# Optimization experiments

Measured on AMD Instinct MI355X. Metric: run time of the kernel, lower is better.

The kernel has to match this reference:

```python
import jax, jax.numpy as jnp
import numpy as np

B, T, D = 2, 2048, 2048
H, HKV, RD = 16, 4, 64
DH = D // H          # 128
REP = H // HKV       # 4
NEG = -1e30


def _apply_rope(x, cos, sin, rd):
    # x: (B, h, T, Dh); cos/sin: (T, rd//2) broadcast over (B, h)
    xr, xp = x[..., :rd], x[..., rd:]
    x1, x2 = xr[..., ::2], xr[..., 1::2]
    rot = jnp.stack([x1 * cos - x2 * sin, x1 * sin + x2 * cos], axis=-1)
    rot = rot.reshape(x1.shape[:-1] + (rd,))
    return jnp.concatenate([rot, xp], axis=-1)


def setup_inputs() -> dict:
    key = jax.random.key(0)
    ks = jax.random.split(key, 6)
    x = jax.random.normal(ks[0], (B, T, D), dtype=jnp.float32)
    # rotary tables for the first RD dims (RD//2 frequency pairs)
    inv_freq = 1.0 / (10000.0 ** (np.arange(RD // 2, dtype=np.float32) / (RD // 2)))
    ang = np.arange(T, dtype=np.float32)[:, None] * inv_freq[None, :]  # (T, RD//2)
    cos = jnp.asarray(np.cos(ang), dtype=jnp.float32)
    sin = jnp.asarray(np.sin(ang), dtype=jnp.float32)
    s = 0.02
    Wq = jax.random.normal(ks[1], (H * DH, D), dtype=jnp.float32) * s
    Wk = jax.random.normal(ks[2], (HKV * DH, D), dtype=jnp.float32) * s
    Wv = jax.random.normal(ks[3], (HKV * DH, D), dtype=jnp.float32) * s
    Wo = jax.random.normal(ks[4], (D, D), dtype=jnp.float32) * s
    temp = jnp.full((H,), 1.0 / np.sqrt(DH), dtype=jnp.float32)
    return {"x": x, "cos": cos, "sin": sin, "Wq": Wq, "Wk": Wk, "Wv": Wv, "Wo": Wo, "temp": temp}


def reference(x, cos, sin, Wq, Wk, Wv, Wo, temp):
    Bt, Tt, _ = x.shape
    q = (x @ Wq.T).reshape(Bt, Tt, H, DH).transpose(0, 2, 1, 3)    # (B,H,T,Dh)
    k = (x @ Wk.T).reshape(Bt, Tt, HKV, DH).transpose(0, 2, 1, 3)  # (B,Hkv,T,Dh)
    v = (x @ Wv.T).reshape(Bt, Tt, HKV, DH).transpose(0, 2, 1, 3)
    k = jnp.repeat(k, REP, axis=1)  # GQA repeat_interleave -> (B,H,T,Dh)
    v = jnp.repeat(v, REP, axis=1)
    q = _apply_rope(q, cos, sin, RD)
    k = _apply_rope(k, cos, sin, RD)
    q = q * temp[None, :, None, None]
    # SDPA causal, with default 1/sqrt(Dh) scale on top of learned temp
    scores = jnp.einsum("bhqd,bhkd->bhqk", q, k) / np.sqrt(DH)
    causal = jnp.tril(jnp.ones((Tt, Tt), dtype=bool))
    scores = jnp.where(causal[None, None], scores, NEG)
    attn = jax.nn.softmax(scores, axis=-1)
    out = jnp.einsum("bhqk,bhkd->bhqd", attn, v)  # (B,H,T,Dh)
    out = out.transpose(0, 2, 1, 3).reshape(Bt, Tt, H * DH)
    return out @ Wo.T
```

## Files before the change

kernel.cpp:

```cpp
#include <hip/hip_runtime.h>
#include <hip/hip_bf16.h>
#include <math.h>

#define B_   2
#define T_   2048
#define D_   2048
#define H_   16
#define HKV_ 4
#define DH_  128
#define RD_  64
#define KD_  (HKV_ * DH_)
#define SQKV 3072
#define VOFF 2560

typedef __attribute__((ext_vector_type(8))) short  short8;
typedef __attribute__((ext_vector_type(4))) short  short4v;
typedef __attribute__((ext_vector_type(4))) float  floatx4;

__device__ __forceinline__ void async16(const __hip_bfloat16* g, __hip_bfloat16* l) {
  __builtin_amdgcn_global_load_lds(
      (const __attribute__((address_space(1))) void*)g,
      (__attribute__((address_space(3))) void*)l, 16, 0, 0);
}

__device__ __forceinline__ short bf16b(float x) {
  union { __hip_bfloat16 h; short s; } u;
  u.h = __float2bfloat16(x);
  return u.s;
}

struct ConvArgs {
  const float* src[5];
  __hip_bfloat16* dst[5];
  int n[5];
};

__global__ __launch_bounds__(256) void conv_bf16(ConvArgs a) {
  const int arr = blockIdx.y;
  const int i = (blockIdx.x * 256 + threadIdx.x) * 8;
  if (i >= a.n[arr]) return;
  const float4 f1 = *(const float4*)(a.src[arr] + i);
  const float4 f2 = *(const float4*)(a.src[arr] + i + 4);
  union { short8 v; __hip_bfloat16 h[8]; } o;
  o.h[0] = __float2bfloat16(f1.x); o.h[1] = __float2bfloat16(f1.y);
  o.h[2] = __float2bfloat16(f1.z); o.h[3] = __float2bfloat16(f1.w);
  o.h[4] = __float2bfloat16(f2.x); o.h[5] = __float2bfloat16(f2.y);
  o.h[6] = __float2bfloat16(f2.z); o.h[7] = __float2bfloat16(f2.w);
  *(short8*)(a.dst[arr] + i) = o.v;
}

template <int MODE>
__global__ __launch_bounds__(512, 2) void gemm_192(const __hip_bfloat16* __restrict__ A,
                                                   const __hip_bfloat16* __restrict__ Bw,
                                                   void* __restrict__ Cout,
                                                   __hip_bfloat16* __restrict__ vtout,
                                                   int M, int N, int K, int nwg_x) {
  __shared__ __hip_bfloat16 ABs[2][28 * 512];

  const int tid  = threadIdx.x;
  const int lane = tid & 63;
  const int w    = tid >> 6;
  const int wm   = w >> 2, wn = w & 3;
  const int quad = lane >> 4, m16 = lane & 15;

  const int nwg = gridDim.x;
  const int q8  = nwg >> 3, r8 = nwg & 7;
  const int xcd = blockIdx.x & 7, o8 = blockIdx.x >> 3;
  const int swz = (xcd < r8 ? xcd * (q8 + 1) : r8 * (q8 + 1) + (xcd - r8) * q8) + o8;
  const int bx = swz % nwg_x, by = swz / nwg_x;
  const int bm = by * 256, bn = bx * 192;

  const __hip_bfloat16* gp[4];
  int lp[4];
  if (w < 7) {
#pragma unroll
    for (int e = 0; e < 4; ++e) {
      const int p = w * 4 + e;
      lp[e] = p * 512;
      if (p < 16) gp[e] = A  + (size_t)(bm + p * 16 + m16) * K + quad * 8;
      else        gp[e] = Bw + (size_t)(bn + (p - 16) * 16 + m16) * K + quad * 8;
    }
  }

  const int nt = K >> 5;

  if (w < 7) {
#pragma unroll
    for (int e = 0; e < 4; ++e) async16(gp[e], &ABs[0][lp[e]]);
  }

  floatx4 acc[8][3] = {};
  const int fragoff = (quad * 16 + m16) * 8;

  for (int t = 0; t < nt; ++t) {
    const int cur = t & 1, stg = cur ^ 1;
    asm volatile("s_waitcnt vmcnt(0)" ::: "memory");
    __builtin_amdgcn_s_barrier();
    __builtin_amdgcn_sched_barrier(0);

    const __hip_bfloat16* base = &ABs[cur][0];
    const bool doStage = (w < 7) && (t + 1 < nt);
    const size_t ko = (size_t)(t + 1) * 32;

    short8 a0[4], b[3];
#pragma unroll
    for (int i = 0; i < 4; ++i)
      a0[i] = *(const short8*)(base + (wm * 8 + i) * 512 + fragoff);
#pragma unroll
    for (int j = 0; j < 3; ++j)
      b[j] = *(const short8*)(base + (16 + wn * 3 + j) * 512 + fragoff);
    if (doStage) {
      async16(gp[0] + ko, &ABs[stg][lp[0]]);
      async16(gp[1] + ko, &ABs[stg][lp[1]]);
    }
    __builtin_amdgcn_s_barrier();
    __builtin_amdgcn_sched_barrier(0);
    __builtin_amdgcn_s_setprio(1);
#pragma unroll
    for (int i = 0; i < 4; ++i)
#pragma unroll
      for (int j = 0; j < 3; ++j)
        acc[i][j] = __builtin_amdgcn_mfma_f32_16x16x32_bf16(a0[i], b[j], acc[i][j], 0, 0, 0);
    __builtin_amdgcn_s_setprio(0);
    __builtin_amdgcn_s_barrier();
    __builtin_amdgcn_sched_barrier(0);

    short8 a1[4];
#pragma unroll
    for (int i = 0; i < 4; ++i)
      a1[i] = *(const short8*)(base + (wm * 8 + 4 + i) * 512 + fragoff);
    if (doStage) {
      async16(gp[2] + ko, &ABs[stg][lp[2]]);
      async16(gp[3] + ko, &ABs[stg][lp[3]]);
    }
    __builtin_amdgcn_s_barrier();
    __builtin_amdgcn_sched_barrier(0);
    __builtin_amdgcn_s_setprio(1);
#pragma unroll
    for (int i = 0; i < 4; ++i)
#pragma unroll
      for (int j = 0; j < 3; ++j)
        acc[4 + i][j] = __builtin_amdgcn_mfma_f32_16x16x32_bf16(a1[i], b[j], acc[4 + i][j], 0, 0, 0);
    __builtin_amdgcn_s_setprio(0);
  }

#pragma unroll
  for (int mt = 0; mt < 8; ++mt)
#pragma unroll
    for (int j = 0; j < 3; ++j) {
      const int col0 = bn + wn * 48 + j * 16;
      const int row0 = bm + wm * 128 + mt * 16 + quad * 4;
      if (MODE == 2 && col0 >= VOFF) {
        const int dh = col0 + m16 - VOFF;
        const int bb = row0 >> 11, t0 = row0 & (T_ - 1);
        short4v pk;
#pragma unroll
        for (int reg = 0; reg < 4; ++reg) pk[reg] = bf16b(acc[mt][j][reg]);
        *(short4v*)&vtout[((size_t)(bb * HKV_ + (dh >> 7)) * DH_ + (dh & 127)) * T_ + t0] = pk;
      } else {
#pragma unroll
        for (int reg = 0; reg < 4; ++reg) {
          const int row = row0 + reg;
          const int col = col0 + m16;
          if (MODE == 0)
            ((float*)Cout)[(size_t)row * N + col] = acc[mt][j][reg];
          else
            ((__hip_bfloat16*)Cout)[(size_t)row * N + col] = __float2bfloat16(acc[mt][j][reg]);
        }
      }
    }
}

__global__ __launch_bounds__(512, 2) void gemm_k1(const __hip_bfloat16* __restrict__ A,
                                                  const __hip_bfloat16* __restrict__ Bw,
                                                  float* __restrict__ Cout,
                                                  int M, int N, int K, int nwg_x) {
  __shared__ __hip_bfloat16 As[3][8 * 512];
  __shared__ __hip_bfloat16 Bs[3][16 * 512];

  const int tid  = threadIdx.x;
  const int lane = tid & 63;
  const int w    = tid >> 6;
  const int wm   = w >> 2, wn = w & 3;
  const int quad = lane >> 4, m16 = lane & 15;

  const int nwg = gridDim.x;
  const int q8  = nwg >> 3, r8 = nwg & 7;
  const int xcd = blockIdx.x & 7, o8 = blockIdx.x >> 3;
  const int swz = (xcd < r8 ? xcd * (q8 + 1) : r8 * (q8 + 1) + (xcd - r8) * q8) + o8;
  const int bx = swz % nwg_x, by = swz / nwg_x;
  const int bm = by * 128, bn = bx * 256;

  const __hip_bfloat16* gA  = A  + (size_t)(bm + w * 16 + m16) * K + quad * 8;
  const __hip_bfloat16* gB0 = Bw + (size_t)(bn + (w * 2 + 0) * 16 + m16) * K + quad * 8;
  const __hip_bfloat16* gB1 = Bw + (size_t)(bn + (w * 2 + 1) * 16 + m16) * K + quad * 8;

  const int nt = K >> 5;

  async16(gA,       &As[0][w * 512]);
  async16(gB0,      &Bs[0][(w * 2 + 0) * 512]);
  async16(gB1,      &Bs[0][(w * 2 + 1) * 512]);
  async16(gA + 32,  &As[1][w * 512]);
  async16(gB0 + 32, &Bs[1][(w * 2 + 0) * 512]);
  async16(gB1 + 32, &Bs[1][(w * 2 + 1) * 512]);

  floatx4 acc[4][4] = {};
  const int fragoff = (quad * 16 + m16) * 8;

  int cur = 0, stg = 2;
  for (int t = 0; t < nt; ++t) {
    if (t < nt - 1) asm volatile("s_waitcnt vmcnt(3)" ::: "memory");
    else            asm volatile("s_waitcnt vmcnt(0)" ::: "memory");
    __builtin_amdgcn_s_barrier();
    __builtin_amdgcn_sched_barrier(0);

    const __hip_bfloat16* abase = &As[cur][0];
    const __hip_bfloat16* bbase = &Bs[cur][0];

    short8 a[4], b[4];
#pragma unroll
    for (int i = 0; i < 4; ++i) {
      a[i] = *(const short8*)(abase + (wm * 4 + i) * 512 + fragoff);
      b[i] = *(const short8*)(bbase + (wn * 4 + i) * 512 + fragoff);
    }
    if (t + 2 < nt) {
      const size_t ko = (size_t)(t + 2) * 32;
      async16(gA + ko,  &As[stg][w * 512]);
      async16(gB0 + ko, &Bs[stg][(w * 2 + 0) * 512]);
      async16(gB1 + ko, &Bs[stg][(w * 2 + 1) * 512]);
    }
    __builtin_amdgcn_s_setprio(1);
#pragma unroll
    for (int i = 0; i < 4; ++i)
#pragma unroll
      for (int j = 0; j < 4; ++j)
        acc[i][j] = __builtin_amdgcn_mfma_f32_16x16x32_bf16(a[i], b[j], acc[i][j], 0, 0, 0);
    __builtin_amdgcn_s_setprio(0);

    cur = (cur == 2) ? 0 : cur + 1;
    stg = (stg == 2) ? 0 : stg + 1;
  }

#pragma unroll
  for (int mi = 0; mi < 4; ++mi)
#pragma unroll
    for (int nj = 0; nj < 4; ++nj)
#pragma unroll
      for (int reg = 0; reg < 4; ++reg) {
        const int row = bm + wm * 64 + mi * 16 + quad * 4 + reg;
        const int col = bn + wn * 64 + nj * 16 + m16;
        Cout[(size_t)row * N + col] = acc[mi][nj][reg];
      }
}

__global__ __launch_bounds__(256) void rope_qk(__hip_bfloat16* __restrict__ qkv,
                                               const float* __restrict__ cosT,
                                               const float* __restrict__ sinT,
                                               const float* __restrict__ temp,
                                               float inv_sqrt_dh) {
  const int unit = blockIdx.x * 4 + (threadIdx.x >> 6);
  const int lane = threadIdx.x & 63;
  const int M = B_ * T_;
  int bt, off;
  float scale;
  if (unit < M * H_) {
    const int h = unit % H_;
    bt = unit / H_;
    off = h * DH_;
    scale = temp[h] * inv_sqrt_dh;
  } else {
    const int u2 = unit - M * H_;
    const int h = u2 % HKV_;
    bt = u2 / HKV_;
    off = D_ + h * DH_;
    scale = 1.0f;
  }
  const int t = bt & (T_ - 1);
  __hip_bfloat16* p = qkv + (size_t)bt * SQKV + off;
  if (lane < 32) {
    const float x1 = __bfloat162float(p[2 * lane]);
    const float x2 = __bfloat162float(p[2 * lane + 1]);
    const float c = cosT[t * (RD_ / 2) + lane];
    const float s = sinT[t * (RD_ / 2) + lane];
    p[2 * lane]     = __float2bfloat16((x1 * c - x2 * s) * scale);
    p[2 * lane + 1] = __float2bfloat16((x1 * s + x2 * c) * scale);
  } else {
    const int d0 = RD_ + (lane - 32) * 2;
    p[d0]     = __float2bfloat16(__bfloat162float(p[d0]) * scale);
    p[d0 + 1] = __float2bfloat16(__bfloat162float(p[d0 + 1]) * scale);
  }
}

__global__ __launch_bounds__(512, 2) void flash_attn_t2(
    const __hip_bfloat16* __restrict__ qkv,
    const __hip_bfloat16* __restrict__ vt,
    __hip_bfloat16* __restrict__ ao) {
  __shared__ __hip_bfloat16 KV[2][16384];

  const int tid = threadIdx.x, lane = tid & 63, w = tid >> 6;
  const int quad = lane >> 4, m16 = lane & 15;

  const int bid = blockIdx.x;
  const int g = bid & 7;
  const int b = g >> 2, kvh = g & 3;
  const int u = bid >> 3;
  const int qt = 63 - u;
  const int hw = w & 3;
  const int khalf = w >> 2;
  const int h = kvh * 4 + hw;
  const int qRow0 = qt * 32;
  const int ktEnd = (qt >> 1) + 1;

  const size_t bT = (size_t)b * T_;

  short8 qa[2][4];
#pragma unroll
  for (int qi = 0; qi < 2; qi++) {
    const __hip_bfloat16* qp = qkv + (bT + qRow0 + qi * 16 + m16) * SQKV + h * DH_;
#pragma unroll
    for (int ks = 0; ks < 4; ks++) qa[qi][ks] = *(const short8*)(qp + ks * 32 + quad * 8);
  }

  const short one = (short)0x3F80;
  const short4v ones4 = {one, one, one, one};

  const __hip_bfloat16* kptr[2];
  const __hip_bfloat16* vptr[2];
#pragma unroll
  for (int e = 0; e < 2; e++) {
    const int I = w * 2 + e;
    const int panelK = I >> 2, kcK = (I & 3) * 4 + quad;
    kptr[e] = qkv + D_ + (bT + panelK * 16 + m16) * SQKV + kvh * DH_ + kcK * 8;
    const int panelV = I >> 1, tc = (I & 1) * 4 + quad;
    vptr[e] = vt + ((size_t)(b * HKV_ + kvh) * DH_ + panelV * 16 + m16) * T_ + tc * 8;
  }

#pragma unroll
  for (int e = 0; e < 2; e++) {
    const int I = w * 2 + e;
    async16(kptr[e], &KV[0][I * 512]);
    async16(vptr[e], &KV[0][8192 + I * 512]);
    kptr[e] += (size_t)64 * SQKV;
    vptr[e] += 64;
  }

  floatx4 ot[8][2] = {};
  floatx4 lt[2] = {};

  for (int kt = 0; kt < ktEnd; kt++) {
    const int cur = kt & 1;
    __syncthreads();
    if (kt + 1 < ktEnd) {
      const int nxt = cur ^ 1;
#pragma unroll
      for (int e = 0; e < 2; e++) {
        const int I = w * 2 + e;
        async16(kptr[e], &KV[nxt][I * 512]);
        async16(vptr[e], &KV[nxt][8192 + I * 512]);
        kptr[e] += (size_t)64 * SQKV;
        vptr[e] += 64;
      }
    }

    const bool last = (kt == ktEnd - 1);
    if (last && khalf == 1 && ((qt & 1) == 0)) continue;

    floatx4 st[2][2] = {};
#pragma unroll
    for (int ki = 0; ki < 2; ki++) {
      const int kg = khalf * 2 + ki;
#pragma unroll
      for (int ks = 0; ks < 4; ks++) {
        const int unit = kg * 256 + (ks * 4 + quad) * 16 + m16;
        const short8 kf = *(const short8*)&KV[cur][unit * 8];
#pragma unroll
        for (int qi = 0; qi < 2; qi++)
          st[ki][qi] = __builtin_amdgcn_mfma_f32_16x16x32_bf16(kf, qa[qi][ks],
                                                               st[ki][qi], 0, 0, 0);
      }
    }

    if (last && khalf == (qt & 1)) {
#pragma unroll
      for (int ki = 0; ki < 2; ki++)
#pragma unroll
        for (int qi = 0; qi < 2; qi++) {
          const int rowg = qRow0 + qi * 16 + m16;
#pragma unroll
          for (int reg = 0; reg < 4; reg++) {
            const int keyg = kt * 64 + khalf * 32 + ki * 16 + quad * 4 + reg;
            if (keyg > rowg) st[ki][qi][reg] = -1e30f;
          }
        }
    }

    short4v pf[2][2];
#pragma unroll
    for (int ki = 0; ki < 2; ki++)
#pragma unroll
      for (int qi = 0; qi < 2; qi++) {
        short4v t;
#pragma unroll
        for (int reg = 0; reg < 4; reg++) t[reg] = bf16b(__expf(st[ki][qi][reg]));
        pf[ki][qi] = t;
      }

#pragma unroll
    for (int mi = 0; mi < 8; mi++)
#pragma unroll
      for (int ki = 0; ki < 2; ki++) {
        const int kg = khalf * 2 + ki;
        const int unit = mi * 128 + (kg * 2 + (quad >> 1)) * 16 + m16;
        const short4v vf = *(const short4v*)&KV[cur][8192 + unit * 8 + (quad & 1) * 4];
#pragma unroll
        for (int qi = 0; qi < 2; qi++)
          ot[mi][qi] = __builtin_amdgcn_mfma_f32_16x16x16bf16_1k(vf, pf[ki][qi],
                                                                 ot[mi][qi], 0, 0, 0);
      }
#pragma unroll
    for (int ki = 0; ki < 2; ki++)
#pragma unroll
      for (int qi = 0; qi < 2; qi++)
        lt[qi] = __builtin_amdgcn_mfma_f32_16x16x16bf16_1k(ones4, pf[ki][qi],
                                                           lt[qi], 0, 0, 0);
  }

  floatx4* scr = (floatx4*)&KV[0][0];
  __syncthreads();
  if (khalf == 1) {
#pragma unroll
    for (int mi = 0; mi < 6; mi++)
#pragma unroll
      for (int qi = 0; qi < 2; qi++)
        scr[((hw * 6 + mi) * 2 + qi) * 64 + lane] = ot[mi][qi];
  }
  __syncthreads();
  if (khalf == 0) {
#pragma unroll
    for (int mi = 0; mi < 6; mi++)
#pragma unroll
      for (int qi = 0; qi < 2; qi++)
        ot[mi][qi] += scr[((hw * 6 + mi) * 2 + qi) * 64 + lane];
  }
  __syncthreads();
  if (khalf == 1) {
#pragma unroll
    for (int j = 0; j < 2; j++)
#pragma unroll
      for (int qi = 0; qi < 2; qi++)
        scr[((hw * 2 + j) * 2 + qi) * 64 + lane] = ot[6 + j][qi];
#pragma unroll
    for (int qi = 0; qi < 2; qi++)
      scr[1024 + (hw * 2 + qi) * 64 + lane] = lt[qi];
  }
  __syncthreads();
  if (khalf == 0) {
#pragma unroll
    for (int j = 0; j < 2; j++)
#pragma unroll
      for (int qi = 0; qi < 2; qi++)
        ot[6 + j][qi] += scr[((hw * 2 + j) * 2 + qi) * 64 + lane];
#pragma unroll
    for (int qi = 0; qi < 2; qi++)
      lt[qi] += scr[1024 + (hw * 2 + qi) * 64 + lane];

#pragma unroll
    for (int qi = 0; qi < 2; qi++) {
      const float inv = 1.0f / lt[qi][0];
      const size_t gr = (bT + qRow0 + qi * 16 + m16) * D_ + h * DH_;
#pragma unroll
      for (int mi = 0; mi < 8; mi++) {
        short4v o;
#pragma unroll
        for (int reg = 0; reg < 4; reg++) o[reg] = bf16b(ot[mi][qi][reg] * inv);
        *(short4v*)&ao[gr + mi * 16 + quad * 4] = o;
      }
    }
  }
}

extern "C" void kernel_launch(void* const* d_in, const int* in_sizes, int n_in,
                              void* d_out, int out_size, void* d_ws, size_t ws_size,
                              hipStream_t stream) {
  const float* x    = (const float*)d_in[0];
  const float* cosT = (const float*)d_in[1];
  const float* sinT = (const float*)d_in[2];
  const float* Wq   = (const float*)d_in[3];
  const float* Wk   = (const float*)d_in[4];
  const float* Wv   = (const float*)d_in[5];
  const float* Wo   = (const float*)d_in[6];
  const float* temp = (const float*)d_in[7];
  float* out = (float*)d_out;

  const int M = B_ * T_;
  const size_t XN   = (size_t)M * D_;
  const size_t WQN  = (size_t)D_ * D_;
  const size_t WKN  = (size_t)KD_ * D_;
  const size_t QKVN = (size_t)M * SQKV;
  const size_t KN   = (size_t)M * KD_;

  __hip_bfloat16* ws = (__hip_bfloat16*)d_ws;
  __hip_bfloat16* xb    = ws;  ws += XN;
  __hip_bfloat16* wqkvb = ws;  ws += WQN + 2 * WKN;
  __hip_bfloat16* wob   = ws;  ws += WQN;
  __hip_bfloat16* qkvb  = ws;  ws += QKVN;
  __hip_bfloat16* vtb   = ws;  ws += KN;
  __hip_bfloat16* aob   = ws;  ws += XN;

  dim3 blk(256);

  ConvArgs ca;
  ca.src[0] = x;  ca.dst[0] = xb;                  ca.n[0] = (int)XN;
  ca.src[1] = Wq; ca.dst[1] = wqkvb;               ca.n[1] = (int)WQN;
  ca.src[2] = Wk; ca.dst[2] = wqkvb + WQN;         ca.n[2] = (int)WKN;
  ca.src[3] = Wv; ca.dst[3] = wqkvb + WQN + WKN;   ca.n[3] = (int)WKN;
  ca.src[4] = Wo; ca.dst[4] = wob;                 ca.n[4] = (int)WQN;
  conv_bf16<<<dim3(4096, 5), blk, 0, stream>>>(ca);

  gemm_192<2><<<dim3((SQKV / 192) * (M / 256)), dim3(512), 0, stream>>>(
      xb, wqkvb, qkvb, vtb, M, SQKV, D_, SQKV / 192);

  const float inv_sqrt_dh = 1.0f / sqrtf((float)DH_);
  rope_qk<<<(M * (H_ + HKV_)) / 4, blk, 0, stream>>>(qkvb, cosT, sinT, temp, inv_sqrt_dh);

  flash_attn_t2<<<512, dim3(512), 0, stream>>>(qkvb, vtb, aob);

  gemm_k1<<<dim3((D_ / 256) * (M / 128)), dim3(512), 0, stream>>>(
      aob, wob, out, M, D_, D_, D_ / 256);
}
```

Before: 327.1 us.

## Fuse RoPE and Q scaling into QKV GEMM epilogue; triple-buffer its LDS

Removes the separate rope_qk kernel and applies rotary embedding plus the temp/sqrt(Dh) scale to Q and K inside the QKV GEMM epilogue. Paired values are exchanged with a lane shuffle, and cos/sin are read from global memory. The GEMM main loop also moves from double to triple LDS buffering with a prefetch distance of two and a partial vmcnt wait. Launch bounds drop from 2 to 1 blocks per CU to make room for the larger LDS footprint. This trades one launch and a read-modify-write pass over Q/K for possibly lower occupancy in the GEMM.

New measurement: 295.8 us. 9.6% less time.

```diff
diff --git a/kernel.cpp b/kernel.cpp
--- a/kernel.cpp
+++ b/kernel.cpp
@@ -50,12 +50,16 @@
 }
 
 template <int MODE>
-__global__ __launch_bounds__(512, 2) void gemm_192(const __hip_bfloat16* __restrict__ A,
+__global__ __launch_bounds__(512, 1) void gemm_192(const __hip_bfloat16* __restrict__ A,
                                                    const __hip_bfloat16* __restrict__ Bw,
                                                    void* __restrict__ Cout,
                                                    __hip_bfloat16* __restrict__ vtout,
+                                                   const float* __restrict__ cosT,
+                                                   const float* __restrict__ sinT,
+                                                   const float* __restrict__ temp,
+                                                   float inv_sqrt_dh,
                                                    int M, int N, int K, int nwg_x) {
-  __shared__ __hip_bfloat16 ABs[2][28 * 512];
+  __shared__ __hip_bfloat16 ABs[3][28 * 512];
 
   const int tid  = threadIdx.x;
   const int lane = tid & 63;
@@ -86,21 +90,24 @@
 
   if (w < 7) {
 #pragma unroll
-    for (int e = 0; e < 4; ++e) async16(gp[e], &ABs[0][lp[e]]);
+    for (int e = 0; e < 4; ++e) async16(gp[e],      &ABs[0][lp[e]]);
+#pragma unroll
+    for (int e = 0; e < 4; ++e) async16(gp[e] + 32, &ABs[1][lp[e]]);
   }
 
   floatx4 acc[8][3] = {};
   const int fragoff = (quad * 16 + m16) * 8;
 
+  int cur = 0, stg = 2;
   for (int t = 0; t < nt; ++t) {
-    const int cur = t & 1, stg = cur ^ 1;
-    asm volatile("s_waitcnt vmcnt(0)" ::: "memory");
+    if (t < nt - 1) asm volatile("s_waitcnt vmcnt(4)" ::: "memory");
+    else            asm volatile("s_waitcnt vmcnt(0)" ::: "memory");
     __builtin_amdgcn_s_barrier();
     __builtin_amdgcn_sched_barrier(0);
 
     const __hip_bfloat16* base = &ABs[cur][0];
-    const bool doStage = (w < 7) && (t + 1 < nt);
-    const size_t ko = (size_t)(t + 1) * 32;
+    const bool doStage = (w < 7) && (t + 2 < nt);
+    const size_t ko = (size_t)(t + 2) * 32;
 
     short8 a0[4], b[3];
 #pragma unroll
@@ -142,6 +149,9 @@
       for (int j = 0; j < 3; ++j)
         acc[4 + i][j] = __builtin_amdgcn_mfma_f32_16x16x32_bf16(a1[i], b[j], acc[4 + i][j], 0, 0, 0);
     __builtin_amdgcn_s_setprio(0);
+
+    cur = (cur == 2) ? 0 : cur + 1;
+    stg = (stg == 2) ? 0 : stg + 1;
   }
 
 #pragma unroll
@@ -158,14 +168,37 @@
         for (int reg = 0; reg < 4; ++reg) pk[reg] = bf16b(acc[mt][j][reg]);
         *(short4v*)&vtout[((size_t)(bb * HKV_ + (dh >> 7)) * DH_ + (dh & 127)) * T_ + t0] = pk;
       } else {
+        float vals[4];
+#pragma unroll
+        for (int reg = 0; reg < 4; ++reg) vals[reg] = acc[mt][j][reg];
+        if (MODE == 2) {
+          const bool isQ   = (col0 < D_);
+          const float scale = isQ ? temp[col0 >> 7] * inv_sqrt_dh : 1.0f;
+          if ((col0 & 127) < 64) {
+            const int iidx = ((col0 & 127) + m16) >> 1;
+            const float sgn = (m16 & 1) ? 1.0f : -1.0f;
+#pragma unroll
+            for (int reg = 0; reg < 4; ++reg) {
+              const int t0 = (row0 + reg) & (T_ - 1);
+              const float c = cosT[t0 * (RD_ / 2) + iidx];
+              const float s = sinT[t0 * (RD_ / 2) + iidx];
+              const float other = __shfl_xor(vals[reg], 1, 64);
+              vals[reg] = vals[reg] * c + sgn * other * s;
+            }
+          }
+          if (isQ) {
+#pragma unroll
+            for (int reg = 0; reg < 4; ++reg) vals[reg] *= scale;
+          }
+        }
 #pragma unroll
         for (int reg = 0; reg < 4; ++reg) {
           const int row = row0 + reg;
           const int col = col0 + m16;
           if (MODE == 0)
-            ((float*)Cout)[(size_t)row * N + col] = acc[mt][j][reg];
+            ((float*)Cout)[(size_t)row * N + col] = vals[reg];
           else
-            ((__hip_bfloat16*)Cout)[(size_t)row * N + col] = __float2bfloat16(acc[mt][j][reg]);
+            ((__hip_bfloat16*)Cout)[(size_t)row * N + col] = __float2bfloat16(vals[reg]);
         }
       }
     }
@@ -251,44 +284,6 @@
         const int col = bn + wn * 64 + nj * 16 + m16;
         Cout[(size_t)row * N + col] = acc[mi][nj][reg];
       }
-}
-
-__global__ __launch_bounds__(256) void rope_qk(__hip_bfloat16* __restrict__ qkv,
-                                               const float* __restrict__ cosT,
-                                               const float* __restrict__ sinT,
-                                               const float* __restrict__ temp,
-                                               float inv_sqrt_dh) {
-  const int unit = blockIdx.x * 4 + (threadIdx.x >> 6);
-  const int lane = threadIdx.x & 63;
-  const int M = B_ * T_;
-  int bt, off;
-  float scale;
-  if (unit < M * H_) {
-    const int h = unit % H_;
-    bt = unit / H_;
-    off = h * DH_;
-    scale = temp[h] * inv_sqrt_dh;
-  } else {
-    const int u2 = unit - M * H_;
-    const int h = u2 % HKV_;
-    bt = u2 / HKV_;
-    off = D_ + h * DH_;
-    scale = 1.0f;
-  }
-  const int t = bt & (T_ - 1);
-  __hip_bfloat16* p = qkv + (size_t)bt * SQKV + off;
-  if (lane < 32) {
-    const float x1 = __bfloat162float(p[2 * lane]);
-    const float x2 = __bfloat162float(p[2 * lane + 1]);
-    const float c = cosT[t * (RD_ / 2) + lane];
-    const float s = sinT[t * (RD_ / 2) + lane];
-    p[2 * lane]     = __float2bfloat16((x1 * c - x2 * s) * scale);
-    p[2 * lane + 1] = __float2bfloat16((x1 * s + x2 * c) * scale);
-  } else {
-    const int d0 = RD_ + (lane - 32) * 2;
-    p[d0]     = __float2bfloat16(__bfloat162float(p[d0]) * scale);
-    p[d0 + 1] = __float2bfloat16(__bfloat162float(p[d0 + 1]) * scale);
-  }
 }
 
 __global__ __launch_bounds__(512, 2) void flash_attn_t2(
@@ -517,11 +512,10 @@
   ca.src[4] = Wo; ca.dst[4] = wob;                 ca.n[4] = (int)WQN;
   conv_bf16<<<dim3(4096, 5), blk, 0, stream>>>(ca);
 
+  const float inv_sqrt_dh = 1.0f / sqrtf((float)DH_);
+
   gemm_192<2><<<dim3((SQKV / 192) * (M / 256)), dim3(512), 0, stream>>>(
-      xb, wqkvb, qkvb, vtb, M, SQKV, D_, SQKV / 192);
-
-  const float inv_sqrt_dh = 1.0f / sqrtf((float)DH_);
-  rope_qk<<<(M * (H_ + HKV_)) / 4, blk, 0, stream>>>(qkvb, cosT, sinT, temp, inv_sqrt_dh);
+      xb, wqkvb, qkvb, vtb, cosT, sinT, temp, inv_sqrt_dh, M, SQKV, D_, SQKV / 192);
 
   flash_attn_t2<<<512, dim3(512), 0, stream>>>(qkvb, vtb, aob);
 
```
